# Kernel optimization log

Hardware: AMD Instinct MI355X
Metric: run time of the kernel (lower is better)

Reference implementation:

```python
import jax, jax.numpy as jnp
import numpy as np

B, P, S, FX, D, DFF, OUT = 8, 10, 160, 11, 64, 256, 1


def _layernorm(h, g, b, eps=1e-6):
    mu = jnp.mean(h, axis=-1, keepdims=True)
    var = jnp.mean(jnp.square(h - mu), axis=-1, keepdims=True)
    return g * (h - mu) * jax.lax.rsqrt(var + eps) + b


def setup_inputs() -> dict:
    key = jax.random.key(0)
    ks = jax.random.split(key, 16)
    n = lambda k, shp, s=0.05: (jax.random.normal(k, shp, jnp.float32) * s)
    return {
        "inputs": jax.random.normal(ks[0], (B, P, S, FX), jnp.float32),
        "targets": jax.random.normal(ks[1], (B, P, S, OUT), jnp.float32),
        "W_proj": n(ks[2], (FX, D)), "b_proj": jnp.zeros((D,), jnp.float32),
        "Wq": n(ks[3], (D, D)), "bq": jnp.zeros((D,), jnp.float32),
        "Wk": n(ks[4], (D, D)), "bk": jnp.zeros((D,), jnp.float32),
        "Wv": n(ks[5], (D, D)), "bv": jnp.zeros((D,), jnp.float32),
        "Wo": n(ks[6], (D, D)), "bo": jnp.zeros((D,), jnp.float32),
        "ln1_g": jnp.ones((D,), jnp.float32), "ln1_b": jnp.zeros((D,), jnp.float32),
        "W1": n(ks[7], (D, DFF)), "b1": jnp.zeros((DFF,), jnp.float32),
        "W2": n(ks[8], (DFF, D)), "b2": jnp.zeros((D,), jnp.float32),
        "ln2_g": jnp.ones((D,), jnp.float32), "ln2_b": jnp.zeros((D,), jnp.float32),
        "Wf": n(ks[9], (D, OUT)), "bf": jnp.zeros((OUT,), jnp.float32),
    }


def reference(inputs, targets, W_proj, b_proj, Wq, bq, Wk, bk, Wv, bv, Wo, bo,
              ln1_g, ln1_b, W1, b1, W2, b2, ln2_g, ln2_b, Wf, bf):
    # inputs: (B,P,S,FX); no-noise (inference/deterministic) SMC-Transformer path:
    # K/V/R resampling is identity, so R_resampl == R.
    d_model = W_proj.shape[1]
    s_len = inputs.shape[2]
    x = (inputs @ W_proj + b_proj) * jnp.sqrt(jnp.float32(d_model))  # (B,P,S,D)
    scale = 1.0 / jnp.sqrt(jnp.float32(d_model))
    pos = jnp.arange(s_len)
    K0 = jnp.zeros(x.shape, jnp.float32)

    def step(carry, inp_t):
        K, V, R = carry
        xt, t = inp_t                                  # xt: (B,P,D), t: scalar
        q = xt @ Wq + bq
        k = xt @ Wk + bk
        v = xt @ Wv + bv
        K = jax.lax.dynamic_update_slice(K, k[:, :, None, :], (0, 0, t, 0))
        V = jax.lax.dynamic_update_slice(V, v[:, :, None, :], (0, 0, t, 0))
        logits = jnp.einsum('bpd,bpsd->bps', q, K) * scale
        logits = jnp.where(pos <= t, logits, jnp.float32(-1e9))  # causal mask
        attn = jax.nn.softmax(logits, axis=-1)                   # (B,P,S)
        z = jnp.einsum('bps,bpsd->bpd', attn, V) @ Wo + bo
        out = _layernorm(z + xt, ln1_g, ln1_b)
        r = jax.nn.relu(out @ W1 + b1) @ W2 + b2                 # pointwise FFN
        r = _layernorm(r + out, ln2_g, ln2_b)
        R = jax.lax.dynamic_update_slice(R, r[:, :, None, :], (0, 0, t, 0))
        return (K, V, R), (r, attn)

    xs = (jnp.transpose(x, (2, 0, 1, 3)), jnp.arange(s_len))
    (K, V, R), (rs, attns) = jax.lax.scan(step, (K0, K0, K0), xs)
    R_out = jnp.transpose(rs, (1, 2, 0, 3))        # (B,P,S,D)
    attn_weights = jnp.transpose(attns, (1, 2, 0, 3))  # (B,P,S,S)
    pred = R_out @ Wf + bf
    pred_resampl = R @ Wf + bf
    return (pred, pred_resampl, K, V, R, attn_weights)
```

## Files before the change

### kernel.cpp

```cpp
#include <hip/hip_runtime.h>
#include <math.h>

#define BB 8
#define PP 10
#define SS 160
#define FXD 11
#define DD 64
#define DFF 256
#define NROW (BB*PP*SS)
#define NBP  (BB*PP)

#define OFF_PRED  0
#define OFF_PREDR 12800
#define OFF_K     25600
#define OFF_V     844800
#define OFF_R     1664000
#define OFF_ATTN  2483200

typedef short short8 __attribute__((ext_vector_type(8)));
typedef float f32x4  __attribute__((ext_vector_type(4)));

__device__ __forceinline__ void fma4(float4& acc, float s, const float4& b){
  acc.x += s*b.x; acc.y += s*b.y; acc.z += s*b.z; acc.w += s*b.w;
}
template<int N>
__device__ __forceinline__ void wred_sum_n(float (&v)[N]){
#pragma unroll
  for (int m = 32; m >= 1; m >>= 1){
#pragma unroll
    for (int i = 0; i < N; ++i) v[i] += __shfl_xor(v[i], m, 64);
  }
}
template<int N>
__device__ __forceinline__ void qred_sum_n(float (&v)[N]){
#pragma unroll
  for (int m = 8; m >= 1; m >>= 1){
#pragma unroll
    for (int i = 0; i < N; ++i) v[i] += __shfl_xor(v[i], m, 64);
  }
}
template<int N>
__device__ __forceinline__ void qred_max_n(float (&v)[N]){
#pragma unroll
  for (int m = 8; m >= 1; m >>= 1){
#pragma unroll
    for (int i = 0; i < N; ++i) v[i] = fmaxf(v[i], __shfl_xor(v[i], m, 64));
  }
}
__device__ __forceinline__ unsigned f2bf(float f){
  unsigned u = __float_as_uint(f);
  return (u + 0x7fffu + ((u >> 16) & 1u)) >> 16;
}
__device__ __forceinline__ unsigned packbf2(float x, float y){
  return f2bf(x) | (f2bf(y) << 16);
}
__device__ __forceinline__ f32x4 mfma16(uint4 a, uint4 b, f32x4 c){
  union { uint4 u; short8 s; } ua, ub;
  ua.u = a; ub.u = b;
  return __builtin_amdgcn_mfma_f32_16x16x32_bf16(ua.s, ub.s, c, 0, 0, 0);
}

__global__ __launch_bounds__(256) void k_pack(
    const float* __restrict__ Wq, const float* __restrict__ Wk,
    const float* __restrict__ Wv, const float* __restrict__ Wo,
    const float* __restrict__ W1, const float* __restrict__ W2,
    unsigned* __restrict__ wp){
  int i = blockIdx.x*256 + threadIdx.x;
  const float* W; int N, K2, base, off;
  if (i < 8192){
    int m = i >> 11; off = i & 2047; N = 64; K2 = 32; base = m*2048;
    W = (m==0)?Wq:((m==1)?Wk:((m==2)?Wv:Wo));
  } else if (i < 16384){
    off = i - 8192; N = 256; K2 = 32; base = 8192; W = W1;
  } else {
    off = i - 16384; N = 64; K2 = 128; base = 16384; W = W2;
  }
  int n = off % N, k2 = off / N;
  wp[base + n*K2 + k2] = packbf2(W[(2*k2)*N + n], W[(2*k2+1)*N + n]);
}

__global__ __launch_bounds__(256) void k_xqkv(const float* __restrict__ inp,
    const float* __restrict__ Wp, const float* __restrict__ bpj,
    const unsigned* __restrict__ wqkvp,
    const float* __restrict__ bq, const float* __restrict__ bk,
    const float* __restrict__ bv,
    float* __restrict__ x, float* __restrict__ Q,
    float* __restrict__ Kc, float* __restrict__ Vc){
  __shared__ __align__(16) float ins[16*12];
  __shared__ __align__(16) unsigned xs2[16*36];
  int tid = threadIdx.x;
  int row0 = blockIdx.x * 16;
  for (int i = tid; i < 16*FXD; i += 256){
    int r = i / FXD, f = i - r*FXD;
    ins[r*12 + f] = inp[row0*FXD + i];
  }
  __syncthreads();
  int tc = tid & 15, tr = tid >> 4;
  {
    float4 a = make_float4(0.f,0.f,0.f,0.f);
#pragma unroll
    for (int f = 0; f < FXD; ++f){
      float v = ins[tr*12 + f];
      float4 w4 = *(const float4*)&Wp[f*64 + tc*4];
      fma4(a, v, w4);
    }
    float4 bp4 = *(const float4*)&bpj[tc*4];
    float4 xv = make_float4((a.x+bp4.x)*8.f, (a.y+bp4.y)*8.f,
                            (a.z+bp4.z)*8.f, (a.w+bp4.w)*8.f);
    *(float4*)&x[(row0+tr)*64 + tc*4] = xv;
    xs2[tr*36 + tc*2]     = packbf2(xv.x, xv.y);
    xs2[tr*36 + tc*2 + 1] = packbf2(xv.z, xv.w);
  }
  __syncthreads();
  int lane = tid & 63, w = tid >> 6;
  int nl = lane & 15, q = lane >> 4;
  uint4 a0 = *(const uint4*)&xs2[nl*36 + q*4];
  uint4 a1 = *(const uint4*)&xs2[nl*36 + 16 + q*4];
  int n = w*16 + nl;
  const float* bias[3] = {bq, bk, bv};
  float* Out[3] = {Q, Kc, Vc};
#pragma unroll
  for (int mat = 0; mat < 3; ++mat){
    const unsigned* wpm = wqkvp + mat*2048;
    uint4 b0 = *(const uint4*)&wpm[n*32 + q*4];
    uint4 b1 = *(const uint4*)&wpm[n*32 + 16 + q*4];
    f32x4 acc = {0.f,0.f,0.f,0.f};
    acc = mfma16(a0, b0, acc);
    acc = mfma16(a1, b1, acc);
    float bvv = bias[mat][n];
    float* O = Out[mat];
#pragma unroll
    for (int r = 0; r < 4; ++r)
      O[(row0 + q*4 + r)*64 + n] = acc[r] + bvv;
  }
}

__global__ __launch_bounds__(256, 4) void k_attn_ffn(const float* __restrict__ Qg,
    const float* __restrict__ Kout, const float* __restrict__ Vout,
    const unsigned* __restrict__ wop,
    const unsigned* __restrict__ w1p, const unsigned* __restrict__ w2p,
    const float* __restrict__ bo,
    const float* __restrict__ g1, const float* __restrict__ b1l,
    const float* __restrict__ x,
    const float* __restrict__ b1, const float* __restrict__ b2,
    const float* __restrict__ g2, const float* __restrict__ b2l,
    const float* __restrict__ Wf, const float* __restrict__ bf,
    float* __restrict__ attn, float* __restrict__ R,
    float* __restrict__ pred, float* __restrict__ predr){
  __shared__ __align__(16) unsigned char smem[35712];
  unsigned* ks2 = (unsigned*)smem;
  unsigned* vs2 = (unsigned*)smem;
  unsigned* as2 = (unsigned*)smem;
  float*    lnb = (float*)(smem + 8448);
  unsigned* qs2 = (unsigned*)(smem + 23040);
  unsigned* os2 = (unsigned*)(smem + 23040);
  unsigned* ps2 = (unsigned*)(smem + 25344);
  float*    zos = (float*)(smem + 25344);
  float*    zs  = (float*)(smem + 30720);
  float*    os  = (float*)(smem + 30720);
  float*    pmax = (float*)(smem + 35072);
  float*    psum = (float*)(smem + 35392);

  int tid = threadIdx.x;
  int bp = blockIdx.x, c = blockIdx.y;
  int t0 = c*16;
  const float* Kb = Kout + bp*(SS*DD);
  const float* Vb = Vout + bp*(SS*DD);
  const float* Qb = Qg + bp*(SS*DD);
  float* Ab = attn + bp*(SS*SS);

  for (int i = tid; i < 2560; i += 256){
    int r = i >> 4, e4 = i & 15;
    float4 kv = *(const float4*)&Kb[r*64 + e4*4];
    unsigned* d = &ks2[r*36 + e4*2];
    d[0] = packbf2(kv.x, kv.y); d[1] = packbf2(kv.z, kv.w);
  }
  for (int i = tid; i < 512; i += 256){
    int r = i >> 5, c2 = i & 31;
    float2 qv = *(const float2*)&Qb[(t0+r)*64 + c2*2];
    qs2[r*36 + c2] = packbf2(qv.x, qv.y);
  }
  __syncthreads();

  int lane = tid & 63, w = tid >> 6;
  int nl = lane & 15, q = lane >> 4;

  int ntiles = (w < 2) ? 3 : 2;
  float lg[3][4], ev[3][4];
  float gm[4], inv[4];
  {
    uint4 aq0 = *(const uint4*)&qs2[nl*36 + q*4];
    uint4 aq1 = *(const uint4*)&qs2[nl*36 + 16 + q*4];
    f32x4 pacc[3];
#pragma unroll
    for (int i = 0; i < 3; ++i){
      pacc[i] = (f32x4){0.f,0.f,0.f,0.f};
      if (i < ntiles){
        int srow = (w + 4*i)*16 + nl;
        uint4 b0 = *(const uint4*)&ks2[srow*36 + q*4];
        uint4 b1 = *(const uint4*)&ks2[srow*36 + 16 + q*4];
        pacc[i] = mfma16(aq0, b0, pacc[i]);
        pacc[i] = mfma16(aq1, b1, pacc[i]);
      }
    }
    float mx[4];
#pragma unroll
    for (int r = 0; r < 4; ++r){
      int t = t0 + q*4 + r;
      float m_ = -INFINITY;
#pragma unroll
      for (int i = 0; i < 3; ++i){
        if (i < ntiles){
          int s = (w + 4*i)*16 + nl;
          float l = (s <= t) ? pacc[i][r]*0.125f : -INFINITY;
          lg[i][r] = l; m_ = fmaxf(m_, l);
        }
      }
      mx[r] = m_;
    }
    qred_max_n<4>(mx);
    if (nl == 0){
#pragma unroll
      for (int r = 0; r < 4; ++r) pmax[(q*4+r)*5 + w] = mx[r];
    }
    __syncthreads();
    float sum[4];
#pragma unroll
    for (int r = 0; r < 4; ++r){
      int row = q*4 + r;
      gm[r] = fmaxf(fmaxf(pmax[row*5+0], pmax[row*5+1]),
                    fmaxf(pmax[row*5+2], pmax[row*5+3]));
      float s_ = 0.f;
#pragma unroll
      for (int i = 0; i < 3; ++i){
        if (i < ntiles){
          ev[i][r] = __expf(lg[i][r] - gm[r]);
          s_ += ev[i][r];
        }
      }
      sum[r] = s_;
    }
    qred_sum_n<4>(sum);
    if (nl == 0){
#pragma unroll
      for (int r = 0; r < 4; ++r) psum[(q*4+r)*5 + w] = sum[r];
    }
    __syncthreads();
#pragma unroll
    for (int r = 0; r < 4; ++r){
      int row = q*4 + r;
      inv[r] = 1.0f / (psum[row*5+0] + psum[row*5+1] +
                       psum[row*5+2] + psum[row*5+3]);
    }
#pragma unroll
    for (int i = 0; i < 3; ++i){
      if (i < ntiles){
        int s = (w + 4*i)*16 + nl;
#pragma unroll
        for (int r = 0; r < 4; ++r){
          int t = t0 + q*4 + r;
          float p = ev[i][r] * inv[r];
          Ab[t*SS + s] = p;
          float pn = __shfl_xor(p, 1, 64);
          if (!(nl & 1))
            ps2[(q*4+r)*84 + (w+4*i)*8 + (nl >> 1)] = packbf2(p, pn);
        }
      }
    }
  }
  __syncthreads();

  for (int i = tid; i < 1280; i += 256){
    int rp = i >> 4, d4 = i & 15;
    float4 v0 = *(const float4*)&Vb[(2*rp)*64 + d4*4];
    float4 v1 = *(const float4*)&Vb[(2*rp+1)*64 + d4*4];
    vs2[(d4*4+0)*84 + rp] = packbf2(v0.x, v1.x);
    vs2[(d4*4+1)*84 + rp] = packbf2(v0.y, v1.y);
    vs2[(d4*4+2)*84 + rp] = packbf2(v0.z, v1.z);
    vs2[(d4*4+3)*84 + rp] = packbf2(v0.w, v1.w);
  }
  __syncthreads();

  {
    f32x4 zacc = {0.f,0.f,0.f,0.f};
#pragma unroll
    for (int ks = 0; ks < 5; ++ks){
      uint4 ap  = *(const uint4*)&ps2[nl*84 + ks*16 + q*4];
      uint4 bv4 = *(const uint4*)&vs2[(w*16+nl)*84 + ks*16 + q*4];
      zacc = mfma16(ap, bv4, zacc);
    }
#pragma unroll
    for (int r = 0; r < 4; ++r)
      zs[(q*4+r)*68 + w*16 + nl] = zacc[r];
  }
  __syncthreads();

  {
    f32x4 cacc = {0.f,0.f,0.f,0.f};
#pragma unroll
    for (int ks = 0; ks < 2; ++ks){
      float4 f0 = *(const float4*)&zs[nl*68 + ks*32 + q*8];
      float4 f1 = *(const float4*)&zs[nl*68 + ks*32 + q*8 + 4];
      uint4 a;
      a.x = packbf2(f0.x, f0.y); a.y = packbf2(f0.z, f0.w);
      a.z = packbf2(f1.x, f1.y); a.w = packbf2(f1.z, f1.w);
      uint4 b = *(const uint4*)&wop[(w*16+nl)*32 + ks*16 + q*4];
      cacc = mfma16(a, b, cacc);
    }
    int col = w*16 + nl;
    float bov = bo[col];
#pragma unroll
    for (int r = 0; r < 4; ++r){
      int row = q*4 + r;
      int grow = bp*SS + t0 + row;
      zos[row*68 + col] = cacc[r] + bov + x[grow*64 + col];
    }
  }
  __syncthreads();

  {
    float h[4], s8v[8];
#pragma unroll
    for (int j = 0; j < 4; ++j){
      int r = w + 4*j;
      h[j] = zos[r*68 + lane];
      s8v[j] = h[j]; s8v[4+j] = h[j]*h[j];
    }
    wred_sum_n<8>(s8v);
    float gl = g1[lane], bl = b1l[lane];
#pragma unroll
    for (int j = 0; j < 4; ++j){
      int r = w + 4*j;
      float mu = s8v[j]*(1.f/64.f);
      float var = s8v[4+j]*(1.f/64.f) - mu*mu;
      float o = gl*(h[j]-mu)*rsqrtf(fmaxf(var,0.f) + 1e-6f) + bl;
      os[r*68 + lane] = o;
      float on = __shfl_xor(o, 1, 64);
      if (!(lane & 1)) os2[r*36 + (lane >> 1)] = packbf2(o, on);
    }
  }
  __syncthreads();

  {
    uint4 ao0 = *(const uint4*)&os2[nl*36 + q*4];
    uint4 ao1 = *(const uint4*)&os2[nl*36 + 16 + q*4];
    f32x4 fa[4];
#pragma unroll
    for (int i = 0; i < 4; ++i){
      fa[i] = (f32x4){0.f,0.f,0.f,0.f};
      int n = (w*4+i)*16 + nl;
      uint4 b0 = *(const uint4*)&w1p[n*32 + q*4];
      uint4 b1v = *(const uint4*)&w1p[n*32 + 16 + q*4];
      fa[i] = mfma16(ao0, b0, fa[i]);
      fa[i] = mfma16(ao1, b1v, fa[i]);
    }
#pragma unroll
    for (int i = 0; i < 4; ++i){
      int n = (w*4+i)*16 + nl;
      float b1b = b1[n];
#pragma unroll
      for (int r = 0; r < 4; ++r){
        float a_ = fmaxf(fa[i][r] + b1b, 0.f);
        float an = __shfl_xor(a_, 1, 64);
        if (!(nl & 1))
          as2[(q*4+r)*132 + w*32 + i*8 + (nl >> 1)] = packbf2(a_, an);
      }
    }
  }
  __syncthreads();

  {
    f32x4 f2 = {0.f,0.f,0.f,0.f};
#pragma unroll
    for (int ks = 0; ks < 8; ++ks){
      uint4 a = *(const uint4*)&as2[nl*132 + ks*16 + q*4];
      uint4 b = *(const uint4*)&w2p[(w*16+nl)*128 + ks*16 + q*4];
      f2 = mfma16(a, b, f2);
    }
    int col = w*16 + nl;
    float b2v = b2[col];
#pragma unroll
    for (int r = 0; r < 4; ++r){
      int row = q*4 + r;
      lnb[row*68 + col] = f2[r] + b2v + os[row*68 + col];
    }
  }
  __syncthreads();

  {
    float wfv = Wf[lane], bfv = bf[0];
    float h[4], s8v[8];
#pragma unroll
    for (int j = 0; j < 4; ++j){
      int r = w*4 + j;
      h[j] = lnb[r*68 + lane];
      s8v[j] = h[j]; s8v[4+j] = h[j]*h[j];
    }
    wred_sum_n<8>(s8v);
    float g2l = g2[lane], b2ll = b2l[lane];
    float pr[4];
#pragma unroll
    for (int j = 0; j < 4; ++j){
      int r = w*4 + j;
      float mu = s8v[j]*(1.f/64.f);
      float var = s8v[4+j]*(1.f/64.f) - mu*mu;
      float rv = g2l*(h[j]-mu)*rsqrtf(fmaxf(var,0.f) + 1e-6f) + b2ll;
      int grow = bp*SS + t0 + r;
      R[grow*64 + lane] = rv;
      pr[j] = rv * wfv;
    }
    wred_sum_n<4>(pr);
    if (lane == 0){
#pragma unroll
      for (int j = 0; j < 4; ++j){
        int grow = bp*SS + t0 + w*4 + j;
        pred[grow]  = pr[j] + bfv;
        predr[grow] = pr[j] + bfv;
      }
    }
  }
}

extern "C" void kernel_launch(void* const* d_in, const int* in_sizes, int n_in,
                              void* d_out, int out_size, void* d_ws, size_t ws_size,
                              hipStream_t stream){
  const float* inputs = (const float*)d_in[0];
  const float* Wp  = (const float*)d_in[2];
  const float* bpj = (const float*)d_in[3];
  const float* Wq  = (const float*)d_in[4];  const float* bq  = (const float*)d_in[5];
  const float* Wk  = (const float*)d_in[6];  const float* bk  = (const float*)d_in[7];
  const float* Wv  = (const float*)d_in[8];  const float* bv  = (const float*)d_in[9];
  const float* Wo  = (const float*)d_in[10]; const float* bo  = (const float*)d_in[11];
  const float* g1  = (const float*)d_in[12]; const float* b1l = (const float*)d_in[13];
  const float* W1  = (const float*)d_in[14]; const float* b1  = (const float*)d_in[15];
  const float* W2  = (const float*)d_in[16]; const float* b2  = (const float*)d_in[17];
  const float* g2  = (const float*)d_in[18]; const float* b2l = (const float*)d_in[19];
  const float* Wf  = (const float*)d_in[20]; const float* bf  = (const float*)d_in[21];

  float* outp = (float*)d_out;
  float* ws   = (float*)d_ws;
  float* x    = ws;
  float* Qw   = ws + 819200;
  unsigned* wpack = (unsigned*)(ws + 1638400);
  const unsigned* wqkvp = wpack;
  const unsigned* wop   = wpack + 6144;
  const unsigned* w1p   = wpack + 8192;
  const unsigned* w2p   = wpack + 16384;

  float* pred  = outp + OFF_PRED;
  float* predr = outp + OFF_PREDR;
  float* Kc    = outp + OFF_K;
  float* Vc    = outp + OFF_V;
  float* Rr    = outp + OFF_R;
  float* attn  = outp + OFF_ATTN;

  k_pack<<<96, 256, 0, stream>>>(Wq, Wk, Wv, Wo, W1, W2, wpack);
  k_xqkv<<<NROW/16, 256, 0, stream>>>(inputs, Wp, bpj, wqkvp, bq, bk, bv,
                                      x, Qw, Kc, Vc);
  k_attn_ffn<<<dim3(NBP, 10), 256, 0, stream>>>(Qw, Kc, Vc, wop, w1p, w2p,
                                                bo, g1, b1l, x, b1, b2,
                                                g2, b2l, Wf, bf,
                                                attn, Rr, pred, predr);
}
```

Baseline: 138.2 us.

## Fold weight packing into projection kernel and stream K/V from global

Removes the separate weight-pack kernel: the projection kernel now packs Wo/W1/W2 to bf16 in its first blocks and converts Wq/Wk/Wv to bf16 fragments directly from global memory. The attention kernel no longer stages full K and V tiles in shared memory; each lane loads and packs its MFMA operands straight from global. The softmax merges max and sum into one barrier using per-wave partial rescaling. Together these drop a launch and two barriers and shrink shared memory, at the cost of redundant strided global loads for V and the weights.

```diff
diff --git a/kernel.cpp b/kernel.cpp
--- a/kernel.cpp
+++ b/kernel.cpp
@@ -59,37 +59,38 @@
   ua.u = a; ub.u = b;
   return __builtin_amdgcn_mfma_f32_16x16x32_bf16(ua.s, ub.s, c, 0, 0, 0);
 }
-
-__global__ __launch_bounds__(256) void k_pack(
-    const float* __restrict__ Wq, const float* __restrict__ Wk,
-    const float* __restrict__ Wv, const float* __restrict__ Wo,
-    const float* __restrict__ W1, const float* __restrict__ W2,
-    unsigned* __restrict__ wp){
-  int i = blockIdx.x*256 + threadIdx.x;
-  const float* W; int N, K2, base, off;
-  if (i < 8192){
-    int m = i >> 11; off = i & 2047; N = 64; K2 = 32; base = m*2048;
-    W = (m==0)?Wq:((m==1)?Wk:((m==2)?Wv:Wo));
-  } else if (i < 16384){
-    off = i - 8192; N = 256; K2 = 32; base = 8192; W = W1;
-  } else {
-    off = i - 16384; N = 64; K2 = 128; base = 16384; W = W2;
-  }
-  int n = off % N, k2 = off / N;
-  wp[base + n*K2 + k2] = packbf2(W[(2*k2)*N + n], W[(2*k2+1)*N + n]);
+__device__ __forceinline__ uint4 pack8(float4 a, float4 b){
+  uint4 r;
+  r.x = packbf2(a.x, a.y); r.y = packbf2(a.z, a.w);
+  r.z = packbf2(b.x, b.y); r.w = packbf2(b.z, b.w);
+  return r;
 }
 
 __global__ __launch_bounds__(256) void k_xqkv(const float* __restrict__ inp,
     const float* __restrict__ Wp, const float* __restrict__ bpj,
-    const unsigned* __restrict__ wqkvp,
-    const float* __restrict__ bq, const float* __restrict__ bk,
-    const float* __restrict__ bv,
+    const float* __restrict__ Wq, const float* __restrict__ bq,
+    const float* __restrict__ Wk, const float* __restrict__ bk,
+    const float* __restrict__ Wv, const float* __restrict__ bv,
+    const float* __restrict__ Wo, const float* __restrict__ W1,
+    const float* __restrict__ W2, unsigned* __restrict__ wpack,
     float* __restrict__ x, float* __restrict__ Q,
     float* __restrict__ Kc, float* __restrict__ Vc){
   __shared__ __align__(16) float ins[16*12];
   __shared__ __align__(16) unsigned xs2[16*36];
   int tid = threadIdx.x;
-  int row0 = blockIdx.x * 16;
+  int g = blockIdx.x;
+  int row0 = g*16;
+  {
+    int pi = g*256 + tid;
+    if (pi < 18432){
+      const float* W; int N, K2, base, off;
+      if (pi < 2048){ W = Wo; N = 64; K2 = 32; base = 0; off = pi; }
+      else if (pi < 10240){ W = W1; N = 256; K2 = 32; base = 2048; off = pi - 2048; }
+      else { W = W2; N = 64; K2 = 128; base = 10240; off = pi - 10240; }
+      int n = off % N, k2 = off / N;
+      wpack[base + n*K2 + k2] = packbf2(W[(2*k2)*N + n], W[(2*k2+1)*N + n]);
+    }
+  }
   for (int i = tid; i < 16*FXD; i += 256){
     int r = i / FXD, f = i - r*FXD;
     ins[r*12 + f] = inp[row0*FXD + i];
@@ -112,18 +113,28 @@
     xs2[tr*36 + tc*2 + 1] = packbf2(xv.z, xv.w);
   }
   __syncthreads();
-  int lane = tid & 63, w = tid >> 6;
-  int nl = lane & 15, q = lane >> 4;
+  int lane = tid & 63, w = tid >> 6, nl = lane & 15, q = lane >> 4;
   uint4 a0 = *(const uint4*)&xs2[nl*36 + q*4];
   uint4 a1 = *(const uint4*)&xs2[nl*36 + 16 + q*4];
   int n = w*16 + nl;
+  const float* Wm[3] = {Wq, Wk, Wv};
   const float* bias[3] = {bq, bk, bv};
   float* Out[3] = {Q, Kc, Vc};
 #pragma unroll
   for (int mat = 0; mat < 3; ++mat){
-    const unsigned* wpm = wqkvp + mat*2048;
-    uint4 b0 = *(const uint4*)&wpm[n*32 + q*4];
-    uint4 b1 = *(const uint4*)&wpm[n*32 + 16 + q*4];
+    const float* W = Wm[mat];
+    float w0 = W[(q*8+0)*64+n], w1 = W[(q*8+1)*64+n];
+    float w2 = W[(q*8+2)*64+n], w3 = W[(q*8+3)*64+n];
+    float w4 = W[(q*8+4)*64+n], w5 = W[(q*8+5)*64+n];
+    float w6 = W[(q*8+6)*64+n], w7 = W[(q*8+7)*64+n];
+    uint4 b0; b0.x = packbf2(w0,w1); b0.y = packbf2(w2,w3);
+    b0.z = packbf2(w4,w5); b0.w = packbf2(w6,w7);
+    float v0 = W[(32+q*8+0)*64+n], v1 = W[(32+q*8+1)*64+n];
+    float v2 = W[(32+q*8+2)*64+n], v3 = W[(32+q*8+3)*64+n];
+    float v4 = W[(32+q*8+4)*64+n], v5 = W[(32+q*8+5)*64+n];
+    float v6 = W[(32+q*8+6)*64+n], v7 = W[(32+q*8+7)*64+n];
+    uint4 b1; b1.x = packbf2(v0,v1); b1.y = packbf2(v2,v3);
+    b1.z = packbf2(v4,v5); b1.w = packbf2(v6,v7);
     f32x4 acc = {0.f,0.f,0.f,0.f};
     acc = mfma16(a0, b0, acc);
     acc = mfma16(a1, b1, acc);
@@ -137,8 +148,7 @@
 
 __global__ __launch_bounds__(256, 4) void k_attn_ffn(const float* __restrict__ Qg,
     const float* __restrict__ Kout, const float* __restrict__ Vout,
-    const unsigned* __restrict__ wop,
-    const unsigned* __restrict__ w1p, const unsigned* __restrict__ w2p,
+    const unsigned* __restrict__ wpack,
     const float* __restrict__ bo,
     const float* __restrict__ g1, const float* __restrict__ b1l,
     const float* __restrict__ x,
@@ -147,19 +157,15 @@
     const float* __restrict__ Wf, const float* __restrict__ bf,
     float* __restrict__ attn, float* __restrict__ R,
     float* __restrict__ pred, float* __restrict__ predr){
-  __shared__ __align__(16) unsigned char smem[35712];
-  unsigned* ks2 = (unsigned*)smem;
-  unsigned* vs2 = (unsigned*)smem;
-  unsigned* as2 = (unsigned*)smem;
-  float*    lnb = (float*)(smem + 8448);
-  unsigned* qs2 = (unsigned*)(smem + 23040);
-  unsigned* os2 = (unsigned*)(smem + 23040);
-  unsigned* ps2 = (unsigned*)(smem + 25344);
-  float*    zos = (float*)(smem + 25344);
-  float*    zs  = (float*)(smem + 30720);
-  float*    os  = (float*)(smem + 30720);
-  float*    pmax = (float*)(smem + 35072);
-  float*    psum = (float*)(smem + 35392);
+  __shared__ __align__(16) unsigned char smA[5376];
+  unsigned* ps2 = (unsigned*)smA;
+  float*    zos = (float*)smA;
+  __shared__ float mws[80], sws[80];
+  __shared__ __align__(16) float zs[16*68];
+  __shared__ __align__(16) float os[16*68];
+  __shared__ __align__(16) unsigned os2[16*36];
+  __shared__ __align__(16) unsigned as2[16*132];
+  __shared__ __align__(16) float lnb[16*68];
 
   int tid = threadIdx.x;
   int bp = blockIdx.x, c = blockIdx.y;
@@ -168,89 +174,78 @@
   const float* Vb = Vout + bp*(SS*DD);
   const float* Qb = Qg + bp*(SS*DD);
   float* Ab = attn + bp*(SS*SS);
-
-  for (int i = tid; i < 2560; i += 256){
-    int r = i >> 4, e4 = i & 15;
-    float4 kv = *(const float4*)&Kb[r*64 + e4*4];
-    unsigned* d = &ks2[r*36 + e4*2];
-    d[0] = packbf2(kv.x, kv.y); d[1] = packbf2(kv.z, kv.w);
-  }
-  for (int i = tid; i < 512; i += 256){
-    int r = i >> 5, c2 = i & 31;
-    float2 qv = *(const float2*)&Qb[(t0+r)*64 + c2*2];
-    qs2[r*36 + c2] = packbf2(qv.x, qv.y);
-  }
-  __syncthreads();
-
-  int lane = tid & 63, w = tid >> 6;
-  int nl = lane & 15, q = lane >> 4;
+  const unsigned* wop = wpack;
+  const unsigned* w1p = wpack + 2048;
+  const unsigned* w2p = wpack + 10240;
+
+  int lane = tid & 63, w = tid >> 6, nl = lane & 15, q = lane >> 4;
 
   int ntiles = (w < 2) ? 3 : 2;
-  float lg[3][4], ev[3][4];
-  float gm[4], inv[4];
-  {
-    uint4 aq0 = *(const uint4*)&qs2[nl*36 + q*4];
-    uint4 aq1 = *(const uint4*)&qs2[nl*36 + 16 + q*4];
+  {
+    const float* qr = &Qb[(t0+nl)*64];
+    uint4 aq0 = pack8(*(const float4*)&qr[q*8],    *(const float4*)&qr[q*8+4]);
+    uint4 aq1 = pack8(*(const float4*)&qr[32+q*8], *(const float4*)&qr[32+q*8+4]);
+    float lg[3][4], ev[3][4];
     f32x4 pacc[3];
 #pragma unroll
     for (int i = 0; i < 3; ++i){
       pacc[i] = (f32x4){0.f,0.f,0.f,0.f};
       if (i < ntiles){
-        int srow = (w + 4*i)*16 + nl;
-        uint4 b0 = *(const uint4*)&ks2[srow*36 + q*4];
-        uint4 b1 = *(const uint4*)&ks2[srow*36 + 16 + q*4];
+        const float* kr = &Kb[((w+4*i)*16 + nl)*64];
+        uint4 b0 = pack8(*(const float4*)&kr[q*8],    *(const float4*)&kr[q*8+4]);
+        uint4 b1 = pack8(*(const float4*)&kr[32+q*8], *(const float4*)&kr[32+q*8+4]);
         pacc[i] = mfma16(aq0, b0, pacc[i]);
         pacc[i] = mfma16(aq1, b1, pacc[i]);
       }
     }
-    float mx[4];
+    float mw_[4];
 #pragma unroll
     for (int r = 0; r < 4; ++r){
       int t = t0 + q*4 + r;
-      float m_ = -INFINITY;
+      float m_ = -1e30f;
 #pragma unroll
       for (int i = 0; i < 3; ++i){
         if (i < ntiles){
           int s = (w + 4*i)*16 + nl;
-          float l = (s <= t) ? pacc[i][r]*0.125f : -INFINITY;
+          float l = (s <= t) ? pacc[i][r]*0.125f : -1e30f;
           lg[i][r] = l; m_ = fmaxf(m_, l);
         }
       }
-      mx[r] = m_;
-    }
-    qred_max_n<4>(mx);
+      mw_[r] = m_;
+    }
+    qred_max_n<4>(mw_);
+    float sw_[4];
+#pragma unroll
+    for (int r = 0; r < 4; ++r){
+      float s_ = 0.f;
+#pragma unroll
+      for (int i = 0; i < 3; ++i){
+        if (i < ntiles){
+          float e = __expf(lg[i][r] - mw_[r]);
+          ev[i][r] = e; s_ += e;
+        }
+      }
+      sw_[r] = s_;
+    }
+    qred_sum_n<4>(sw_);
     if (nl == 0){
 #pragma unroll
-      for (int r = 0; r < 4; ++r) pmax[(q*4+r)*5 + w] = mx[r];
+      for (int r = 0; r < 4; ++r){
+        mws[(q*4+r)*5 + w] = mw_[r];
+        sws[(q*4+r)*5 + w] = sw_[r];
+      }
     }
     __syncthreads();
-    float sum[4];
+    float scale[4];
 #pragma unroll
     for (int r = 0; r < 4; ++r){
       int row = q*4 + r;
-      gm[r] = fmaxf(fmaxf(pmax[row*5+0], pmax[row*5+1]),
-                    fmaxf(pmax[row*5+2], pmax[row*5+3]));
-      float s_ = 0.f;
-#pragma unroll
-      for (int i = 0; i < 3; ++i){
-        if (i < ntiles){
-          ev[i][r] = __expf(lg[i][r] - gm[r]);
-          s_ += ev[i][r];
-        }
-      }
-      sum[r] = s_;
-    }
-    qred_sum_n<4>(sum);
-    if (nl == 0){
-#pragma unroll
-      for (int r = 0; r < 4; ++r) psum[(q*4+r)*5 + w] = sum[r];
-    }
-    __syncthreads();
-#pragma unroll
-    for (int r = 0; r < 4; ++r){
-      int row = q*4 + r;
-      inv[r] = 1.0f / (psum[row*5+0] + psum[row*5+1] +
-                       psum[row*5+2] + psum[row*5+3]);
+      float m0 = mws[row*5+0], m1 = mws[row*5+1];
+      float m2 = mws[row*5+2], m3 = mws[row*5+3];
+      float gm = fmaxf(fmaxf(m0,m1), fmaxf(m2,m3));
+      float tot = sws[row*5+0]*__expf(m0-gm) + sws[row*5+1]*__expf(m1-gm)
+                + sws[row*5+2]*__expf(m2-gm) + sws[row*5+3]*__expf(m3-gm);
+      scale[r] = __expf(mw_[r]-gm) / tot;
     }
 #pragma unroll
     for (int i = 0; i < 3; ++i){
@@ -258,40 +253,34 @@
         int s = (w + 4*i)*16 + nl;
 #pragma unroll
         for (int r = 0; r < 4; ++r){
-          int t = t0 + q*4 + r;
-          float p = ev[i][r] * inv[r];
-          Ab[t*SS + s] = p;
-          float pn = __shfl_xor(p, 1, 64);
+          float p_ = ev[i][r] * scale[r];
+          Ab[(t0 + q*4 + r)*SS + s] = p_;
+          float pn = __shfl_xor(p_, 1, 64);
           if (!(nl & 1))
-            ps2[(q*4+r)*84 + (w+4*i)*8 + (nl >> 1)] = packbf2(p, pn);
+            ps2[(q*4+r)*84 + (w+4*i)*8 + (nl >> 1)] = packbf2(p_, pn);
         }
       }
     }
   }
   __syncthreads();
 
-  for (int i = tid; i < 1280; i += 256){
-    int rp = i >> 4, d4 = i & 15;
-    float4 v0 = *(const float4*)&Vb[(2*rp)*64 + d4*4];
-    float4 v1 = *(const float4*)&Vb[(2*rp+1)*64 + d4*4];
-    vs2[(d4*4+0)*84 + rp] = packbf2(v0.x, v1.x);
-    vs2[(d4*4+1)*84 + rp] = packbf2(v0.y, v1.y);
-    vs2[(d4*4+2)*84 + rp] = packbf2(v0.z, v1.z);
-    vs2[(d4*4+3)*84 + rp] = packbf2(v0.w, v1.w);
-  }
-  __syncthreads();
-
-  {
+  {
+    int d = w*16 + nl;
     f32x4 zacc = {0.f,0.f,0.f,0.f};
 #pragma unroll
     for (int ks = 0; ks < 5; ++ks){
-      uint4 ap  = *(const uint4*)&ps2[nl*84 + ks*16 + q*4];
-      uint4 bv4 = *(const uint4*)&vs2[(w*16+nl)*84 + ks*16 + q*4];
-      zacc = mfma16(ap, bv4, zacc);
+      int sb = ks*32 + q*8;
+      uint4 bv;
+      bv.x = packbf2(Vb[(sb+0)*64+d], Vb[(sb+1)*64+d]);
+      bv.y = packbf2(Vb[(sb+2)*64+d], Vb[(sb+3)*64+d]);
+      bv.z = packbf2(Vb[(sb+4)*64+d], Vb[(sb+5)*64+d]);
+      bv.w = packbf2(Vb[(sb+6)*64+d], Vb[(sb+7)*64+d]);
+      uint4 ap = *(const uint4*)&ps2[nl*84 + ks*16 + q*4];
+      zacc = mfma16(ap, bv, zacc);
     }
 #pragma unroll
     for (int r = 0; r < 4; ++r)
-      zs[(q*4+r)*68 + w*16 + nl] = zacc[r];
+      zs[(q*4+r)*68 + d] = zacc[r];
   }
   __syncthreads();
 
@@ -301,9 +290,7 @@
     for (int ks = 0; ks < 2; ++ks){
       float4 f0 = *(const float4*)&zs[nl*68 + ks*32 + q*8];
       float4 f1 = *(const float4*)&zs[nl*68 + ks*32 + q*8 + 4];
-      uint4 a;
-      a.x = packbf2(f0.x, f0.y); a.y = packbf2(f0.z, f0.w);
-      a.z = packbf2(f1.x, f1.y); a.w = packbf2(f1.z, f1.w);
+      uint4 a = pack8(f0, f1);
       uint4 b = *(const uint4*)&wop[(w*16+nl)*32 + ks*16 + q*4];
       cacc = mfma16(a, b, cacc);
     }
@@ -442,10 +429,6 @@
   float* x    = ws;
   float* Qw   = ws + 819200;
   unsigned* wpack = (unsigned*)(ws + 1638400);
-  const unsigned* wqkvp = wpack;
-  const unsigned* wop   = wpack + 6144;
-  const unsigned* w1p   = wpack + 8192;
-  const unsigned* w2p   = wpack + 16384;
 
   float* pred  = outp + OFF_PRED;
   float* predr = outp + OFF_PREDR;
@@ -454,10 +437,9 @@
   float* Rr    = outp + OFF_R;
   float* attn  = outp + OFF_ATTN;
 
-  k_pack<<<96, 256, 0, stream>>>(Wq, Wk, Wv, Wo, W1, W2, wpack);
-  k_xqkv<<<NROW/16, 256, 0, stream>>>(inputs, Wp, bpj, wqkvp, bq, bk, bv,
-                                      x, Qw, Kc, Vc);
-  k_attn_ffn<<<dim3(NBP, 10), 256, 0, stream>>>(Qw, Kc, Vc, wop, w1p, w2p,
+  k_xqkv<<<NROW/16, 256, 0, stream>>>(inputs, Wp, bpj, Wq, bq, Wk, bk, Wv, bv,
+                                      Wo, W1, W2, wpack, x, Qw, Kc, Vc);
+  k_attn_ffn<<<dim3(NBP, 10), 256, 0, stream>>>(Qw, Kc, Vc, wpack,
                                                 bo, g1, b1l, x, b1, b2,
                                                 g2, b2l, Wf, bf,
                                                 attn, Rr, pred, predr);
```

After: 131.6 us. 4.8% less time.
